# Kernel tuning notes

Measured on AMD Instinct MI355X. Metric: run time of the kernel, lower is better.

## Reference

```python
import jax, jax.numpy as jnp
import numpy as np

B, Cin, H, W = 8, 256, 32, 32
KS, NH, K = 32, 8, 5          # key_size == value_size, num_heads, kernel_size
STRIDE, PAD = 1, 2
Cout = KS * 3 * NH            # 768
EPS = 1e-5


def setup_inputs() -> dict:
    key = jax.random.key(0)
    k0, k1, k2 = jax.random.split(key, 3)
    return {
        "x": jax.random.normal(k0, (B, Cin, H, W), jnp.float32),
        "conv_w": jax.random.normal(k1, (Cout, Cin), jnp.float32) / np.sqrt(Cin).astype(np.float32),
        "conv_b": jax.random.normal(k2, (Cout,), jnp.float32) * 0.02,
        "gn_w": jnp.ones((Cout,), jnp.float32),
        "gn_b": jnp.zeros((Cout,), jnp.float32),
    }


def reference(x, conv_w, conv_b, gn_w, gn_b):
    Bb = x.shape[0]
    OH = (H + 2 * PAD - K) // STRIDE + 1
    OW = (W + 2 * PAD - K) // STRIDE + 1

    # 1x1 conv: (B, Cout, H, W)
    attn = jnp.einsum('bchw,oc->bohw', x, conv_w) + conv_b[None, :, None, None]

    # unfold / Tile2d -> (B, KH, KW, Cout, OH, OW)
    ap = jnp.pad(attn, ((0, 0), (0, 0), (PAD, PAD), (PAD, PAD)))
    rows = []
    for kh in range(K):
        cols = [ap[:, :, kh:kh + OH * STRIDE:STRIDE, kw:kw + OW * STRIDE:STRIDE]
                for kw in range(K)]
        rows.append(jnp.stack(cols, axis=1))          # (B, KW, C, OH, OW)
    tiles = jnp.stack(rows, axis=1)                   # (B, KH, KW, C, OH, OW)

    # GroupNorm over (group_channels, OH, OW) per (b, kh, kw) sample.
    # groups = 3*NH, group size = KS (each head's key/query/value chunk).
    G = 3 * NH
    t = tiles.reshape(Bb, K, K, G, KS, OH, OW)
    mean = t.mean(axis=(4, 5, 6), keepdims=True)
    var = t.var(axis=(4, 5, 6), keepdims=True)        # biased, like torch GroupNorm
    t = (t - mean) * jax.lax.rsqrt(var + EPS)
    t = t.reshape(Bb, K, K, Cout, OH, OW)
    t = t * gn_w[None, None, None, :, None, None] + gn_b[None, None, None, :, None, None]

    # (B, OH, OW, NH, 3*KS, KH*KW)
    t = t.transpose(0, 4, 5, 3, 1, 2).reshape(Bb, OH, OW, NH, 3 * KS, K * K)
    keyt = t[..., :KS, :]            # (B, OH, OW, NH, KS, KK)
    qt = t[..., KS:2 * KS, :]
    vt = t[..., 2 * KS:, :]          # (B, OH, OW, NH, VS, KK)

    q = qt.mean(axis=-1)             # mean query over the window: (B, OH, OW, NH, KS)
    sal = jnp.einsum('bijnk,bijnkp->bijnp', q, keyt) / np.float32(np.sqrt(KS))
    mask = jax.nn.softmax(sal, axis=-1)               # (B, OH, OW, NH, KK)
    out = jnp.einsum('bijnvp,bijnp->bijnv', vt, mask)  # (B, OH, OW, NH, VS)

    out = out.transpose(0, 3, 4, 1, 2).reshape(Bb, NH * KS, OH, OW)
    return out
```

## Files before the change

### kernel.cpp

```cpp
#include <hip/hip_runtime.h>
#include <hip/hip_bf16.h>

#define B_    8
#define CIN   256
#define COUT  768
#define G_    24
#define PW    40
#define PLANE 1440
#define EPS_  1e-5f

typedef float f32x4 __attribute__((ext_vector_type(4)));
typedef short s16x8 __attribute__((ext_vector_type(8)));
typedef unsigned short ushort_t;
typedef unsigned short u16x4 __attribute__((ext_vector_type(4)));
typedef unsigned long long ull_t;

#define LDS_FENCE() do { asm volatile("" ::: "memory"); \
                         __builtin_amdgcn_s_waitcnt(0xC07F); \
                         asm volatile("" ::: "memory"); } while (0)

static __device__ __forceinline__ ushort_t f2bf(float f) {
    union { float f; unsigned u; } a; a.f = f;
    const unsigned u = a.u;
    const unsigned r = u + 0x7FFFu + ((u >> 16) & 1u);
    return (ushort_t)(r >> 16);
}
static __device__ __forceinline__ float bf2f(ushort_t h) {
    union { unsigned u; float f; } a; a.u = ((unsigned)h) << 16; return a.f;
}
static __device__ __forceinline__ void st4(float* dst, u16x4 v) {
    *(f32x4*)dst = f32x4{ bf2f(v[0]), bf2f(v[1]), bf2f(v[2]), bf2f(v[3]) };
}

__launch_bounds__(256)
__global__ void prep(const float* __restrict__ x, const float* __restrict__ w,
                     ushort_t* __restrict__ Xt, ushort_t* __restrict__ Wt) {
    const int z = blockIdx.x;
    const int t = threadIdx.x;
    if (z < 2048) {
        __shared__ ushort_t tile[32][33];
        const int b  = z >> 8, rem = z & 255;
        const int k0 = (rem >> 5) * 32, n0 = (rem & 31) * 32;
        const int kk = t >> 5, nn = t & 31;
        #pragma unroll
        for (int it = 0; it < 4; ++it) {
            const int kr = kk + it * 8;
            tile[kr][nn] = f2bf(x[((size_t)(b * 256 + k0 + kr)) * 1024 + n0 + nn]);
        }
        __syncthreads();
        const int kk2 = t & 31, nb = t >> 5;
        #pragma unroll
        for (int it = 0; it < 4; ++it) {
            const int nr = nb + it * 8;
            Xt[((size_t)(b * 1024 + n0 + nr)) * 256 + k0 + kk2] = tile[kk2][nr];
        }
    } else {
        const int idx = (z - 2048) * 256 + t;
        Wt[idx] = f2bf(w[idx]);
    }
}

__launch_bounds__(256)
__global__ void conv_gemm(const ushort_t* __restrict__ Wt, const ushort_t* __restrict__ Xt,
                          const float* __restrict__ bias, ushort_t* __restrict__ attn,
                          float* __restrict__ rowAgg) {
    const int t = threadIdx.x;
    const int wv = t >> 6, lane = t & 63;
    const int q = lane >> 4, l15 = lane & 15;
    const int m0 = blockIdx.y * 64;
    const int mw = wv * 16;
    const int n_t = blockIdx.x * 64;
    const int b = n_t >> 10, nl0 = n_t & 1023;
    const int y0 = nl0 >> 5;

    __shared__ ushort_t Ct[64][2][44];
    __shared__ float red[128][11];

    const ushort_t* aP = Wt + (size_t)(m0 + mw + l15) * 256 + q * 8;
    const ushort_t* bP = Xt + (size_t)(b * 1024 + nl0 + l15) * 256 + q * 8;

    f32x4 acc[4] = {{0,0,0,0},{0,0,0,0},{0,0,0,0},{0,0,0,0}};
    #pragma unroll
    for (int k0 = 0; k0 < 256; k0 += 32) {
        const s16x8 a  = *(const s16x8*)(aP + k0);
        const s16x8 b0 = *(const s16x8*)(bP + k0);
        const s16x8 b1 = *(const s16x8*)(bP + 16 * 256 + k0);
        const s16x8 b2 = *(const s16x8*)(bP + 32 * 256 + k0);
        const s16x8 b3 = *(const s16x8*)(bP + 48 * 256 + k0);
        acc[0] = __builtin_amdgcn_mfma_f32_16x16x32_bf16(a, b0, acc[0], 0, 0, 0);
        acc[1] = __builtin_amdgcn_mfma_f32_16x16x32_bf16(a, b1, acc[1], 0, 0, 0);
        acc[2] = __builtin_amdgcn_mfma_f32_16x16x32_bf16(a, b2, acc[2], 0, 0, 0);
        acc[3] = __builtin_amdgcn_mfma_f32_16x16x32_bf16(a, b3, acc[3], 0, 0, 0);
    }

    float bb[4];
    #pragma unroll
    for (int r = 0; r < 4; ++r) bb[r] = bias[m0 + mw + q * 4 + r];
    #pragma unroll
    for (int j = 0; j < 4; ++j) {
        const int yy = j >> 1, xx = (j & 1) * 16 + l15;
        #pragma unroll
        for (int r = 0; r < 4; ++r)
            Ct[mw + q * 4 + r][yy][2 + xx] = f2bf(acc[j][r] + bb[r]);
    }
    #pragma unroll
    for (int it = 0; it < 2; ++it) {
        const int id = it * 256 + t;
        const int m = id >> 3, yy = (id >> 2) & 1, pos = id & 3;
        const int us = (pos == 0) ? 0 : (32 + 2 * pos);
        *(unsigned*)&Ct[m][yy][us] = 0u;
    }
    __syncthreads();

    ushort_t* pb = attn + ((size_t)(b * COUT + m0)) * PLANE;
    #pragma unroll
    for (int it = 0; it < 5; ++it) {
        const int id = it * 256 + t;
        const int m = id / 20, rem = id % 20, yy = rem / 10, s = rem % 10;
        const ull_t v = *(const ull_t*)&Ct[m][yy][s * 4];
        *(ull_t*)(pb + (size_t)m * PLANE + (y0 + yy + 2) * PW + s * 4) = v;
    }
    if (y0 == 0 || y0 == 30) {
        const int rowA = (y0 == 0) ? 0 : 34;
        #pragma unroll
        for (int it = 0; it < 5; ++it) {
            const int id = it * 256 + t;
            const int m = id / 20, rem = id % 20, yy = rem / 10, s = rem % 10;
            *(ull_t*)(pb + (size_t)m * PLANE + (rowA + yy) * PW + s * 4) = 0ull;
        }
    }

    if (t < 128) {
        const int gi = t >> 6, yy = (t >> 5) & 1, c = t & 31;
        const int m = gi * 32 + c;
        float lin = 0.f, sq = 0.f, e0 = 0.f, e1 = 0.f, e30 = 0.f, e31 = 0.f;
        #pragma unroll
        for (int u = 0; u < 9; ++u) {
            const ull_t vv = *(const ull_t*)&Ct[m][yy][u * 4];
            const unsigned lo = (unsigned)vv, hi = (unsigned)(vv >> 32);
            union { unsigned u; float f; } f0, f1, f2, f3;
            f0.u = lo << 16; f1.u = lo & 0xffff0000u;
            f2.u = hi << 16; f3.u = hi & 0xffff0000u;
            lin += (f0.f + f1.f) + (f2.f + f3.f);
            sq  += (f0.f * f0.f + f1.f * f1.f) + (f2.f * f2.f + f3.f * f3.f);
            if (u == 0) { e0 = f2.f; e1 = f3.f; }
            if (u == 8) { e30 = f0.f; e31 = f1.f; }
        }
        red[t][0] = lin; red[t][1] = sq;
        red[t][2] = e0;  red[t][3] = e0 * e0;
        red[t][4] = e1;  red[t][5] = e1 * e1;
        red[t][6] = e30; red[t][7] = e30 * e30;
        red[t][8] = e31; red[t][9] = e31 * e31;
    }
    __syncthreads();
    if (t < 40) {
        const int s = t % 10, gy = t / 10;
        const int gi = gy >> 1, yy = gy & 1;
        float sum = 0.f;
        #pragma unroll
        for (int c = 0; c < 32; ++c) sum += red[gi * 64 + yy * 32 + c][s];
        const int g = blockIdx.y * 2 + gi;
        rowAgg[(((size_t)b * G_ + g) * 32 + (y0 + yy)) * 10 + s] = sum;
    }
}

__launch_bounds__(64)
__global__ void gnfin(const float* __restrict__ rowAgg,
                      float* __restrict__ meanArr, float* __restrict__ rstdArr) {
    const int bg = blockIdx.x;
    const int t = threadIdx.x;
    __shared__ float rp[32][5], rp2[32][5];
    if (t < 32) {
        const float* a = rowAgg + ((size_t)bg * 32 + t) * 10;
        const float S = a[0], Sq = a[1];
        const float e0 = a[2], q0 = a[3], e1 = a[4], q1 = a[5];
        const float e30 = a[6], q30 = a[7], e31 = a[8], q31 = a[9];
        rp[t][0] = S - e30 - e31; rp[t][1] = S - e31; rp[t][2] = S;
        rp[t][3] = S - e0;        rp[t][4] = S - e0 - e1;
        rp2[t][0] = Sq - q30 - q31; rp2[t][1] = Sq - q31; rp2[t][2] = Sq;
        rp2[t][3] = Sq - q0;        rp2[t][4] = Sq - q0 - q1;
    }
    __syncthreads();
    if (t < 25) {
        const int kw = t % 5, kh = t / 5;
        float cs = 0.f, cs2 = 0.f;
        #pragma unroll
        for (int yy = 0; yy < 32; ++yy) { cs += rp[yy][kw]; cs2 += rp2[yy][kw]; }
        if (kh == 0)      { cs -= rp[30][kw] + rp[31][kw]; cs2 -= rp2[30][kw] + rp2[31][kw]; }
        else if (kh == 1) { cs -= rp[31][kw];              cs2 -= rp2[31][kw]; }
        else if (kh == 3) { cs -= rp[0][kw];               cs2 -= rp2[0][kw]; }
        else if (kh == 4) { cs -= rp[0][kw] + rp[1][kw];   cs2 -= rp2[0][kw] + rp2[1][kw]; }
        const float inv_n = 1.f / 32768.f;
        const float mean = cs * inv_n;
        const float var  = cs2 * inv_n - mean * mean;
        meanArr[bg * 25 + t] = mean;
        rstdArr[bg * 25 + t] = rsqrtf(var + EPS_);
    }
}

__launch_bounds__(64)
__global__ void local_attn(const ushort_t* __restrict__ attn,
                           const float* __restrict__ meanArr, const float* __restrict__ rstdArr,
                           const float* __restrict__ gn_w, const float* __restrict__ gn_b,
                           float* __restrict__ out) {
    const int blk = blockIdx.x;
    const int b = blk >> 8;
    const int n = (blk >> 5) & 7;
    const int i0 = blk & 31;
    const int t = threadIdx.x;
    const int h = t >> 5;
    const int j = t & 31;

    __shared__ float KB[2][2][208];
    __shared__ float QB[2][2][208];
    __shared__ float s_rq[25], s_mq[25], s_rk[25], s_ck[25], s_rv[25], s_cv[25];
    __shared__ float s_gw[96], s_gb[96];

    if (t < 25) {
        const int gk = (b * G_ + n * 3) * 25 + t;
        const float mK = meanArr[gk],      rK = rstdArr[gk];
        const float mQ = meanArr[gk + 25], rQ = rstdArr[gk + 25];
        const float mV = meanArr[gk + 50], rV = rstdArr[gk + 50];
        s_rk[t] = rK; s_ck[t] = mK * rK;
        s_rq[t] = rQ; s_mq[t] = mQ * rQ;
        s_rv[t] = rV; s_cv[t] = mV * rV;
    }
    s_gw[t] = gn_w[n * 96 + t];
    s_gb[t] = gn_b[n * 96 + t];
    if (t < 32) {
        s_gw[64 + t] = gn_w[n * 96 + 64 + t];
        s_gb[64 + t] = gn_b[n * 96 + 64 + t];
    }
    __syncthreads();

    float rq[25]; float cQ = 0.f;
    #pragma unroll
    for (int p = 0; p < 25; ++p) { rq[p] = s_rq[p]; cQ += s_mq[p]; }

    const ushort_t* regB = attn + (size_t)(b * COUT + n * 96) * PLANE + i0 * PW;
    const bool stg = (j < 25);
    const int eo1 = j * 4, eo2 = (j + 25) * 4;

    const ushort_t* baseK = regB + (size_t)(h * 16) * PLANE;
    const ushort_t* baseQ = regB + (size_t)(32 + h * 16) * PLANE;
    const ushort_t* baseV = regB + (size_t)(64 + h * 16) * PLANE;

    u16x4 nK1{0,0,0,0}, nK2{0,0,0,0}, nQ1{0,0,0,0}, nQ2{0,0,0,0};
    u16x4 fK1{0,0,0,0}, fK2{0,0,0,0}, fQ1{0,0,0,0}, fQ2{0,0,0,0};
    if (stg) {
        const u16x4 a1 = *(const u16x4*)(baseK + eo1), a2 = *(const u16x4*)(baseK + eo2);
        const u16x4 q1 = *(const u16x4*)(baseQ + eo1), q2 = *(const u16x4*)(baseQ + eo2);
        st4(&KB[h][0][eo1], a1); st4(&KB[h][0][eo2], a2);
        st4(&QB[h][0][eo1], q1); st4(&QB[h][0][eo2], q2);
        nK1 = *(const u16x4*)(baseK + PLANE + eo1); nK2 = *(const u16x4*)(baseK + PLANE + eo2);
        nQ1 = *(const u16x4*)(baseQ + PLANE + eo1); nQ2 = *(const u16x4*)(baseQ + PLANE + eo2);
        fK1 = *(const u16x4*)(baseK + 2 * (size_t)PLANE + eo1);
        fK2 = *(const u16x4*)(baseK + 2 * (size_t)PLANE + eo2);
        fQ1 = *(const u16x4*)(baseQ + 2 * (size_t)PLANE + eo1);
        fQ2 = *(const u16x4*)(baseQ + 2 * (size_t)PLANE + eo2);
    }
    LDS_FENCE();

    float sal[25];
    #pragma unroll
    for (int p = 0; p < 25; ++p) sal[p] = 0.f;
    float sumQ2 = 0.f, sumQB = 0.f;

    for (int cc = 0; cc < 16; ++cc) {
        const int buf = cc & 1;
        if (stg && cc < 15) {
            st4(&KB[h][buf ^ 1][eo1], nK1); st4(&KB[h][buf ^ 1][eo2], nK2);
            st4(&QB[h][buf ^ 1][eo1], nQ1); st4(&QB[h][buf ^ 1][eo2], nQ2);
            nK1 = fK1; nK2 = fK2; nQ1 = fQ1; nQ2 = fQ2;
            if (cc < 13) {
                fK1 = *(const u16x4*)(baseK + (size_t)(cc + 3) * PLANE + eo1);
                fK2 = *(const u16x4*)(baseK + (size_t)(cc + 3) * PLANE + eo2);
                fQ1 = *(const u16x4*)(baseQ + (size_t)(cc + 3) * PLANE + eo1);
                fQ2 = *(const u16x4*)(baseQ + (size_t)(cc + 3) * PLANE + eo2);
            } else if (cc == 13) {
                fK1 = *(const u16x4*)(baseV + eo1);
                fK2 = *(const u16x4*)(baseV + eo2);
                fQ1 = *(const u16x4*)(baseV + (size_t)PLANE + eo1);
                fQ2 = *(const u16x4*)(baseV + (size_t)PLANE + eo2);
            }
        }
        const int ch = h * 16 + cc;
        const float* qb = &QB[h][buf][j];
        const float* kb = &KB[h][buf][j];
        float qa0 = 0.f, qa1 = 0.f, qa2 = 0.f, qa3 = 0.f, qa4 = 0.f;
        #pragma unroll
        for (int kw = 0; kw < 5; ++kw) {
            qa0 += rq[0 * 5 + kw] * qb[0 * PW + kw];
            qa1 += rq[1 * 5 + kw] * qb[1 * PW + kw];
            qa2 += rq[2 * 5 + kw] * qb[2 * PW + kw];
            qa3 += rq[3 * 5 + kw] * qb[3 * PW + kw];
            qa4 += rq[4 * 5 + kw] * qb[4 * PW + kw];
        }
        const float qa = (qa0 + qa1) + (qa2 + qa3) + qa4;
        const float qk  = s_gw[32 + ch] * ((qa - cQ) * 0.04f) + s_gb[32 + ch];
        const float qk2 = qk * s_gw[ch];
        sumQ2 += qk2; sumQB += qk * s_gb[ch];
        #pragma unroll
        for (int kh = 0; kh < 5; ++kh)
            #pragma unroll
            for (int kw = 0; kw < 5; ++kw)
                sal[kh * 5 + kw] += qk2 * kb[kh * PW + kw];
        LDS_FENCE();
    }

    u16x4 vA1 = nQ1, vA2 = nQ2, vB1{0,0,0,0}, vB2{0,0,0,0};
    if (stg) {
        st4(&KB[h][0][eo1], nK1); st4(&KB[h][0][eo2], nK2);
        vB1 = *(const u16x4*)(baseV + 2 * (size_t)PLANE + eo1);
        vB2 = *(const u16x4*)(baseV + 2 * (size_t)PLANE + eo2);
    }

    sumQ2 += __shfl_xor(sumQ2, 32);
    sumQB += __shfl_xor(sumQB, 32);
    #pragma unroll
    for (int p = 0; p < 25; ++p) sal[p] += __shfl_xor(sal[p], 32);

    #pragma unroll
    for (int p = 0; p < 25; ++p) sal[p] = s_rk[p] * sal[p] - s_ck[p] * sumQ2 + sumQB;

    const float scale = 0.17677669529663687f;
    float mmax = -3.4e38f;
    #pragma unroll
    for (int p = 0; p < 25; ++p) { sal[p] *= scale; mmax = fmaxf(mmax, sal[p]); }
    float ssum = 0.f;
    #pragma unroll
    for (int p = 0; p < 25; ++p) { sal[p] = __expf(sal[p] - mmax); ssum += sal[p]; }
    const float rs = 1.f / ssum;
    float cV2 = 0.f;
    #pragma unroll
    for (int p = 0; p < 25; ++p) {
        const float m = sal[p] * rs;
        sal[p] = m * s_rv[p];
        cV2 += m * s_cv[p];
    }
    LDS_FENCE();

    for (int cc = 0; cc < 16; ++cc) {
        const int buf = cc & 1;
        if (stg && cc < 15) {
            st4(&KB[h][buf ^ 1][eo1], vA1); st4(&KB[h][buf ^ 1][eo2], vA2);
            vA1 = vB1; vA2 = vB2;
            if (cc < 13) {
                vB1 = *(const u16x4*)(baseV + (size_t)(cc + 3) * PLANE + eo1);
                vB2 = *(const u16x4*)(baseV + (size_t)(cc + 3) * PLANE + eo2);
            }
        }
        const int v = h * 16 + cc;
        const float* vb = &KB[h][buf][j];
        float a0 = 0.f, a1 = 0.f, a2 = 0.f, a3 = 0.f, a4 = 0.f;
        #pragma unroll
        for (int kw = 0; kw < 5; ++kw) {
            a0 += sal[0 * 5 + kw] * vb[0 * PW + kw];
            a1 += sal[1 * 5 + kw] * vb[1 * PW + kw];
            a2 += sal[2 * 5 + kw] * vb[2 * PW + kw];
            a3 += sal[3 * 5 + kw] * vb[3 * PW + kw];
            a4 += sal[4 * 5 + kw] * vb[4 * PW + kw];
        }
        const float acc = (a0 + a1) + (a2 + a3) + a4;
        out[((size_t)(b * 256 + n * 32 + v) * 32 + i0) * 32 + j] =
            s_gw[64 + v] * acc + (s_gb[64 + v] - s_gw[64 + v] * cV2);
        LDS_FENCE();
    }
}

extern "C" void kernel_launch(void* const* d_in, const int* in_sizes, int n_in,
                              void* d_out, int out_size, void* d_ws, size_t ws_size,
                              hipStream_t stream) {
    const float* x      = (const float*)d_in[0];
    const float* conv_w = (const float*)d_in[1];
    const float* conv_b = (const float*)d_in[2];
    const float* gn_w   = (const float*)d_in[3];
    const float* gn_b   = (const float*)d_in[4];
    float* out = (float*)d_out;

    ushort_t* attn    = (ushort_t*)d_ws;
    ushort_t* Xt      = attn + 8847360;
    ushort_t* Wt      = Xt + 2097152;
    float*    rowAgg  = (float*)(Wt + 196608);
    float*    meanArr = rowAgg + 61440;
    float*    rstdArr = meanArr + 4800;

    prep<<<2816, 256, 0, stream>>>(x, conv_w, Xt, Wt);
    conv_gemm<<<dim3(128, 12), 256, 0, stream>>>(Wt, Xt, conv_b, attn, rowAgg);
    gnfin<<<192, 64, 0, stream>>>(rowAgg, meanArr, rstdArr);
    local_attn<<<2048, 64, 0, stream>>>(attn, meanArr, rstdArr, gn_w, gn_b, out);
}
```

Before: 132.6 us.

## Fuse bf16 conversion and transpose of inputs into the conv GEMM kernel

Removes the separate prep kernel that transposed x and converted x and the weights to bf16. The GEMM now loads fp32 x directly, packs it to bf16 into a transposed shared-memory tile, and converts weight rows to bf16 in registers before the MFMAs. The shared tile is reused as the later Ct and red buffers, with an added barrier. This saves one launch and a round trip of intermediate data through memory. In exchange, each of the 12 row-blocks repeats the x conversion and each column-block repeats the weight conversion, and loads are now fp32.

```diff
diff --git a/kernel.cpp b/kernel.cpp
--- a/kernel.cpp
+++ b/kernel.cpp
@@ -31,37 +31,12 @@
 static __device__ __forceinline__ void st4(float* dst, u16x4 v) {
     *(f32x4*)dst = f32x4{ bf2f(v[0]), bf2f(v[1]), bf2f(v[2]), bf2f(v[3]) };
 }
+static __device__ __forceinline__ unsigned pk2(float lo, float hi) {
+    return (unsigned)f2bf(lo) | ((unsigned)f2bf(hi) << 16);
+}
 
 __launch_bounds__(256)
-__global__ void prep(const float* __restrict__ x, const float* __restrict__ w,
-                     ushort_t* __restrict__ Xt, ushort_t* __restrict__ Wt) {
-    const int z = blockIdx.x;
-    const int t = threadIdx.x;
-    if (z < 2048) {
-        __shared__ ushort_t tile[32][33];
-        const int b  = z >> 8, rem = z & 255;
-        const int k0 = (rem >> 5) * 32, n0 = (rem & 31) * 32;
-        const int kk = t >> 5, nn = t & 31;
-        #pragma unroll
-        for (int it = 0; it < 4; ++it) {
-            const int kr = kk + it * 8;
-            tile[kr][nn] = f2bf(x[((size_t)(b * 256 + k0 + kr)) * 1024 + n0 + nn]);
-        }
-        __syncthreads();
-        const int kk2 = t & 31, nb = t >> 5;
-        #pragma unroll
-        for (int it = 0; it < 4; ++it) {
-            const int nr = nb + it * 8;
-            Xt[((size_t)(b * 1024 + n0 + nr)) * 256 + k0 + kk2] = tile[kk2][nr];
-        }
-    } else {
-        const int idx = (z - 2048) * 256 + t;
-        Wt[idx] = f2bf(w[idx]);
-    }
-}
-
-__launch_bounds__(256)
-__global__ void conv_gemm(const ushort_t* __restrict__ Wt, const ushort_t* __restrict__ Xt,
+__global__ void conv_gemm(const float* __restrict__ wsrc, const float* __restrict__ x,
                           const float* __restrict__ bias, ushort_t* __restrict__ attn,
                           float* __restrict__ rowAgg) {
     const int t = threadIdx.x;
@@ -73,25 +48,52 @@
     const int b = n_t >> 10, nl0 = n_t & 1023;
     const int y0 = nl0 >> 5;
 
-    __shared__ ushort_t Ct[64][2][44];
-    __shared__ float red[128][11];
-
-    const ushort_t* aP = Wt + (size_t)(m0 + mw + l15) * 256 + q * 8;
-    const ushort_t* bP = Xt + (size_t)(b * 1024 + nl0 + l15) * 256 + q * 8;
+    __shared__ ushort_t Bs[64][264];
+    ushort_t (*Ct)[2][44] = (ushort_t (*)[2][44])(&Bs[0][0]);
+    float (*red)[11]      = (float (*)[11])((char*)(&Bs[0][0]) + 64 * 2 * 44 * 2);
+
+    {
+        const int half = t >> 7;
+        const int kp = t & 127;
+        const int k2 = kp * 2;
+        const float* xr0 = x + (size_t)b * (CIN * 1024) + (size_t)k2 * 1024 + nl0 + half * 32;
+        const float* xr1 = xr0 + 1024;
+        #pragma unroll
+        for (int c = 0; c < 8; ++c) {
+            const float4 u0 = *(const float4*)(xr0 + c * 4);
+            const float4 u1 = *(const float4*)(xr1 + c * 4);
+            const int nn = half * 32 + c * 4;
+            *(unsigned*)&Bs[nn + 0][k2] = pk2(u0.x, u1.x);
+            *(unsigned*)&Bs[nn + 1][k2] = pk2(u0.y, u1.y);
+            *(unsigned*)&Bs[nn + 2][k2] = pk2(u0.z, u1.z);
+            *(unsigned*)&Bs[nn + 3][k2] = pk2(u0.w, u1.w);
+        }
+    }
+    __syncthreads();
+
+    const float* aPf = wsrc + (size_t)(m0 + mw + l15) * 256 + q * 8;
 
     f32x4 acc[4] = {{0,0,0,0},{0,0,0,0},{0,0,0,0},{0,0,0,0}};
     #pragma unroll
     for (int k0 = 0; k0 < 256; k0 += 32) {
-        const s16x8 a  = *(const s16x8*)(aP + k0);
-        const s16x8 b0 = *(const s16x8*)(bP + k0);
-        const s16x8 b1 = *(const s16x8*)(bP + 16 * 256 + k0);
-        const s16x8 b2 = *(const s16x8*)(bP + 32 * 256 + k0);
-        const s16x8 b3 = *(const s16x8*)(bP + 48 * 256 + k0);
+        const float4 af0 = *(const float4*)(aPf + k0);
+        const float4 af1 = *(const float4*)(aPf + k0 + 4);
+        s16x8 a;
+        a[0] = (short)f2bf(af0.x); a[1] = (short)f2bf(af0.y);
+        a[2] = (short)f2bf(af0.z); a[3] = (short)f2bf(af0.w);
+        a[4] = (short)f2bf(af1.x); a[5] = (short)f2bf(af1.y);
+        a[6] = (short)f2bf(af1.z); a[7] = (short)f2bf(af1.w);
+        const int kk = k0 + q * 8;
+        const s16x8 b0 = *(const s16x8*)&Bs[l15 +  0][kk];
+        const s16x8 b1 = *(const s16x8*)&Bs[l15 + 16][kk];
+        const s16x8 b2 = *(const s16x8*)&Bs[l15 + 32][kk];
+        const s16x8 b3 = *(const s16x8*)&Bs[l15 + 48][kk];
         acc[0] = __builtin_amdgcn_mfma_f32_16x16x32_bf16(a, b0, acc[0], 0, 0, 0);
         acc[1] = __builtin_amdgcn_mfma_f32_16x16x32_bf16(a, b1, acc[1], 0, 0, 0);
         acc[2] = __builtin_amdgcn_mfma_f32_16x16x32_bf16(a, b2, acc[2], 0, 0, 0);
         acc[3] = __builtin_amdgcn_mfma_f32_16x16x32_bf16(a, b3, acc[3], 0, 0, 0);
     }
+    __syncthreads();
 
     float bb[4];
     #pragma unroll
@@ -379,14 +381,11 @@
     float* out = (float*)d_out;
 
     ushort_t* attn    = (ushort_t*)d_ws;
-    ushort_t* Xt      = attn + 8847360;
-    ushort_t* Wt      = Xt + 2097152;
-    float*    rowAgg  = (float*)(Wt + 196608);
+    float*    rowAgg  = (float*)(attn + 8847360);
     float*    meanArr = rowAgg + 61440;
     float*    rstdArr = meanArr + 4800;
 
-    prep<<<2816, 256, 0, stream>>>(x, conv_w, Xt, Wt);
-    conv_gemm<<<dim3(128, 12), 256, 0, stream>>>(Wt, Xt, conv_b, attn, rowAgg);
+    conv_gemm<<<dim3(128, 12), 256, 0, stream>>>(conv_w, x, conv_b, attn, rowAgg);
     gnfin<<<192, 64, 0, stream>>>(rowAgg, meanArr, rstdArr);
     local_attn<<<2048, 64, 0, stream>>>(attn, meanArr, rstdArr, gn_w, gn_b, out);
 }
```

New measurement: 122.3 us. 1.08x faster.
